# Kernel optimization log

Hardware: AMD Instinct MI355X
Metric: run time of the kernel (lower is better)

Reference implementation:

```python
import jax, jax.numpy as jnp
import numpy as np

N_CLASSES = 91

def setup_inputs() -> dict:
    key = jax.random.key(0)
    k1, k2 = jax.random.split(key)
    B, H, W = 32, 1024, 1024
    inputs = jax.random.randint(k1, (B, H, W), 0, N_CLASSES, dtype=jnp.int32)
    targets = jax.random.randint(k2, (B, H, W), 0, N_CLASSES, dtype=jnp.int32)
    smooth = jnp.ones((1,), dtype=jnp.float32)  # original default smooth=1
    return {"inputs": inputs, "targets": targets, "smooth": smooth}

def reference(inputs, targets, smooth):
    # Single-pass histogram formulation of the original 91-iteration loop.
    B = inputs.shape[0]
    x = inputs.reshape(B, -1)   # [B, N] int labels
    t = targets.reshape(B, -1)  # [B, N]
    rows = jnp.arange(B)[:, None]
    # per-class counts: cnt_x[b,c] = #pixels with x==c (== a.sum per class)
    cnt_x = jnp.zeros((B, N_CLASSES), jnp.float32).at[rows, x].add(1.0)
    cnt_t = jnp.zeros((B, N_CLASSES), jnp.float32).at[rows, t].add(1.0)
    # intersection[b,c] = #pixels with x==t==c; route mismatches to a dump bin
    match = jnp.where(x == t, x, N_CLASSES)
    inter = jnp.zeros((B, N_CLASSES + 1), jnp.float32).at[rows, match].add(1.0)[:, :N_CLASSES]
    union = cnt_x + cnt_t - inter  # total - intersection
    s = smooth[0]
    iou = (inter + s) / (union + s)  # [B, C]
    return iou.mean(axis=1)          # sum_IoU / n_classes, shape [B]
```

## Files before the change

kernel.cpp:

```cpp
#include <hip/hip_runtime.h>

#define NC 91
#define NB 32
#define HW (1024 * 1024)
#define PIX_PER_BLOCK 4096

__device__ __forceinline__ void proc_pixel(int x, int t, int* s_u, int* s_i) {
    atomicAdd(&s_u[x], 1);
    if (x != t) {
        atomicAdd(&s_u[t], 1);
    } else {
        atomicAdd(&s_i[x], 1);
    }
}

__global__ __launch_bounds__(256) void hist_kernel(const int* __restrict__ x,
                                                   const int* __restrict__ t,
                                                   int* __restrict__ g_inter,
                                                   int* __restrict__ g_union) {
    __shared__ int s_i[NC];
    __shared__ int s_u[NC];
    const int tid = threadIdx.x;
    if (tid < NC) { s_i[tid] = 0; s_u[tid] = 0; }
    __syncthreads();

    const int b = blockIdx.y;
    const long base = (long)b * HW + (long)blockIdx.x * PIX_PER_BLOCK;
    const int4* __restrict__ x4 = (const int4*)(x + base);
    const int4* __restrict__ t4 = (const int4*)(t + base);

#pragma unroll
    for (int i = 0; i < 4; ++i) {
        int4 xv = x4[i * 256 + tid];
        int4 tv = t4[i * 256 + tid];
        proc_pixel(xv.x, tv.x, s_u, s_i);
        proc_pixel(xv.y, tv.y, s_u, s_i);
        proc_pixel(xv.z, tv.z, s_u, s_i);
        proc_pixel(xv.w, tv.w, s_u, s_i);
    }
    __syncthreads();

    if (tid < NC) {
        int u = s_u[tid];
        int in = s_i[tid];
        if (u)  atomicAdd(&g_union[b * NC + tid], u);
        if (in) atomicAdd(&g_inter[b * NC + tid], in);
    }
}

__global__ __launch_bounds__(64) void finalize_kernel(const int* __restrict__ g_inter,
                                                      const int* __restrict__ g_union,
                                                      const float* __restrict__ smooth,
                                                      float* __restrict__ out) {
    const int b = blockIdx.x;
    const int lane = threadIdx.x;
    const float s = smooth[0];
    float acc = 0.0f;
    for (int c = lane; c < NC; c += 64) {
        float in = (float)g_inter[b * NC + c];
        float un = (float)g_union[b * NC + c];
        acc += (in + s) / (un + s);
    }
#pragma unroll
    for (int off = 32; off > 0; off >>= 1)
        acc += __shfl_down(acc, off, 64);
    if (lane == 0) out[b] = acc / (float)NC;
}

extern "C" void kernel_launch(void* const* d_in, const int* in_sizes, int n_in,
                              void* d_out, int out_size, void* d_ws, size_t ws_size,
                              hipStream_t stream) {
    const int* x = (const int*)d_in[0];
    const int* t = (const int*)d_in[1];
    const float* smooth = (const float*)d_in[2];
    float* out = (float*)d_out;

    int* g_inter = (int*)d_ws;
    int* g_union = g_inter + NB * NC;

    hipMemsetAsync(d_ws, 0, 2 * NB * NC * sizeof(int), stream);

    dim3 grid(HW / PIX_PER_BLOCK, NB);
    hist_kernel<<<grid, 256, 0, stream>>>(x, t, g_inter, g_union);
    finalize_kernel<<<NB, 64, 0, stream>>>(g_inter, g_union, smooth, out);
}
```

Measured before the change: 276.6 us.

## Privatize LDS histograms per wave and column with branchless merged bins

Replaces the two shared 91-entry histograms with one 182-bin histogram. Bin c holds union counts and bin 91+c holds intersection counts, and each pixel's second bin is chosen by a select instead of a divergent branch. Each wave gets its own copy of the histogram, split into 8 interleaved columns by lane, so that fewer lanes contend for the same LDS address in atomics. In exchange, the kernel uses more LDS (about 23 KB per block), adds a zeroing loop, and adds a final 32-way reduction per bin before the global atomics.

```diff
diff --git a/kernel.cpp b/kernel.cpp
--- a/kernel.cpp
+++ b/kernel.cpp
@@ -1,28 +1,25 @@
 #include <hip/hip_runtime.h>
 
 #define NC 91
+#define NBIN 182
+#define NCOL 8
 #define NB 32
 #define HW (1024 * 1024)
 #define PIX_PER_BLOCK 4096
 
-__device__ __forceinline__ void proc_pixel(int x, int t, int* s_u, int* s_i) {
-    atomicAdd(&s_u[x], 1);
-    if (x != t) {
-        atomicAdd(&s_u[t], 1);
-    } else {
-        atomicAdd(&s_i[x], 1);
-    }
-}
-
 __global__ __launch_bounds__(256) void hist_kernel(const int* __restrict__ x,
                                                    const int* __restrict__ t,
-                                                   int* __restrict__ g_inter,
-                                                   int* __restrict__ g_union) {
-    __shared__ int s_i[NC];
-    __shared__ int s_u[NC];
+                                                   int* __restrict__ g_hist) {
+    __shared__ int s_h[4][NBIN * NCOL];
+
     const int tid = threadIdx.x;
-    if (tid < NC) { s_i[tid] = 0; s_u[tid] = 0; }
+    int* sf = &s_h[0][0];
+    for (int i = tid; i < 4 * NBIN * NCOL; i += 256) sf[i] = 0;
     __syncthreads();
+
+    const int wave = tid >> 6;
+    const int col  = tid & (NCOL - 1);
+    int* h = s_h[wave];
 
     const int b = blockIdx.y;
     const long base = (long)b * HW + (long)blockIdx.x * PIX_PER_BLOCK;
@@ -33,23 +30,34 @@
     for (int i = 0; i < 4; ++i) {
         int4 xv = x4[i * 256 + tid];
         int4 tv = t4[i * 256 + tid];
-        proc_pixel(xv.x, tv.x, s_u, s_i);
-        proc_pixel(xv.y, tv.y, s_u, s_i);
-        proc_pixel(xv.z, tv.z, s_u, s_i);
-        proc_pixel(xv.w, tv.w, s_u, s_i);
+        int b0 = xv.x, b1 = xv.y, b2 = xv.z, b3 = xv.w;
+        int c0 = (xv.x == tv.x) ? (NC + xv.x) : tv.x;
+        int c1 = (xv.y == tv.y) ? (NC + xv.y) : tv.y;
+        int c2 = (xv.z == tv.z) ? (NC + xv.z) : tv.z;
+        int c3 = (xv.w == tv.w) ? (NC + xv.w) : tv.w;
+        atomicAdd(&h[b0 * NCOL + col], 1);
+        atomicAdd(&h[c0 * NCOL + col], 1);
+        atomicAdd(&h[b1 * NCOL + col], 1);
+        atomicAdd(&h[c1 * NCOL + col], 1);
+        atomicAdd(&h[b2 * NCOL + col], 1);
+        atomicAdd(&h[c2 * NCOL + col], 1);
+        atomicAdd(&h[b3 * NCOL + col], 1);
+        atomicAdd(&h[c3 * NCOL + col], 1);
     }
     __syncthreads();
 
-    if (tid < NC) {
-        int u = s_u[tid];
-        int in = s_i[tid];
-        if (u)  atomicAdd(&g_union[b * NC + tid], u);
-        if (in) atomicAdd(&g_inter[b * NC + tid], in);
+    for (int c = tid; c < NBIN; c += 256) {
+        int s = 0;
+#pragma unroll
+        for (int w = 0; w < 4; ++w) {
+#pragma unroll
+            for (int k = 0; k < NCOL; ++k) s += s_h[w][c * NCOL + k];
+        }
+        if (s) atomicAdd(&g_hist[b * NBIN + c], s);
     }
 }
 
-__global__ __launch_bounds__(64) void finalize_kernel(const int* __restrict__ g_inter,
-                                                      const int* __restrict__ g_union,
+__global__ __launch_bounds__(64) void finalize_kernel(const int* __restrict__ g_hist,
                                                       const float* __restrict__ smooth,
                                                       float* __restrict__ out) {
     const int b = blockIdx.x;
@@ -57,8 +65,8 @@
     const float s = smooth[0];
     float acc = 0.0f;
     for (int c = lane; c < NC; c += 64) {
-        float in = (float)g_inter[b * NC + c];
-        float un = (float)g_union[b * NC + c];
+        float un = (float)g_hist[b * NBIN + c];
+        float in = (float)g_hist[b * NBIN + NC + c];
         acc += (in + s) / (un + s);
     }
 #pragma unroll
@@ -75,12 +83,11 @@
     const float* smooth = (const float*)d_in[2];
     float* out = (float*)d_out;
 
-    int* g_inter = (int*)d_ws;
-    int* g_union = g_inter + NB * NC;
+    int* g_hist = (int*)d_ws;
 
-    hipMemsetAsync(d_ws, 0, 2 * NB * NC * sizeof(int), stream);
+    hipMemsetAsync(d_ws, 0, NB * NBIN * sizeof(int), stream);
 
     dim3 grid(HW / PIX_PER_BLOCK, NB);
-    hist_kernel<<<grid, 256, 0, stream>>>(x, t, g_inter, g_union);
-    finalize_kernel<<<NB, 64, 0, stream>>>(g_inter, g_union, smooth, out);
+    hist_kernel<<<grid, 256, 0, stream>>>(x, t, g_hist);
+    finalize_kernel<<<NB, 64, 0, stream>>>(g_hist, smooth, out);
 }
```

After: 281.3 us. No clear change (+1.7%).
